# Performance work log

Hardware: AMD Instinct MI355X
Metric: run time of the kernel (lower is better)

## Reference

```python
import jax, jax.numpy as jnp
import numpy as np

L, D, H, HID, V, MAXLEN = 4, 768, 12, 3072, 32000, 1024
HD = D // H

def _pe_table(max_len, d_model):
    pos = np.arange(max_len)[:, None].astype(np.float64)
    i = np.arange(d_model)[None, :]
    ang = pos / np.power(10000.0, 2 * (i // 2) / d_model)
    ang[:, 0::2] = np.sin(ang[:, 0::2])
    ang[:, 1::2] = np.cos(ang[:, 1::2])
    return jnp.asarray(ang, dtype=jnp.float32)

def _layernorm(x, g, b, eps=1e-5):
    mu = jnp.mean(x, axis=-1, keepdims=True)
    var = jnp.mean(jnp.square(x - mu), axis=-1, keepdims=True)
    return (x - mu) * jax.lax.rsqrt(var + eps) * g + b

def setup_inputs() -> dict:
    key = jax.random.key(0)
    ks = jax.random.split(key, 16)
    s = 0.02
    inp = {
        'tokens': jax.random.randint(ks[0], (4, 1024), 0, V),
        'emb': jax.random.normal(ks[1], (V, D), jnp.float32) * s,
        'pe': _pe_table(MAXLEN, D),
        'ln1_g': jnp.ones((L, D), jnp.float32), 'ln1_b': jnp.zeros((L, D), jnp.float32),
        'wq': jax.random.normal(ks[2], (L, D, D), jnp.float32) * s, 'bq': jnp.zeros((L, D), jnp.float32),
        'wk': jax.random.normal(ks[3], (L, D, D), jnp.float32) * s, 'bk': jnp.zeros((L, D), jnp.float32),
        'wv': jax.random.normal(ks[4], (L, D, D), jnp.float32) * s, 'bv': jnp.zeros((L, D), jnp.float32),
        'wo': jax.random.normal(ks[5], (L, D, D), jnp.float32) * s, 'bo': jnp.zeros((L, D), jnp.float32),
        'ln2_g': jnp.ones((L, D), jnp.float32), 'ln2_b': jnp.zeros((L, D), jnp.float32),
        'w1': jax.random.normal(ks[6], (L, D, HID), jnp.float32) * s, 'b1': jnp.zeros((L, HID), jnp.float32),
        'w2': jax.random.normal(ks[7], (L, HID, D), jnp.float32) * s, 'b2': jnp.zeros((L, D), jnp.float32),
        'lnf_g': jnp.ones((D,), jnp.float32), 'lnf_b': jnp.zeros((D,), jnp.float32),
        'w_out': jax.random.normal(ks[8], (D, V), jnp.float32) * s,
    }
    return inp

def reference(tokens, emb, pe, ln1_g, ln1_b, wq, bq, wk, bk, wv, bv, wo, bo, ln2_g, ln2_b, w1, b1, w2, b2, lnf_g, lnf_b, w_out):
    B, S = tokens.shape
    x = emb[tokens] + pe[:S]  # [B,S,D]
    causal = jnp.tril(jnp.ones((S, S), bool))  # True = keep
    scale = 1.0 / jnp.sqrt(jnp.float32(D))  # NOTE: module scales by sqrt(d_model), not sqrt(head_dim)
    for l in range(L):
        h = _layernorm(x, ln1_g[l], ln1_b[l])
        def heads(w, b):
            return (h @ w + b).reshape(B, S, H, HD).transpose(0, 2, 1, 3)  # [B,H,S,HD]
        q, k, v = heads(wq[l], bq[l]), heads(wk[l], bk[l]), heads(wv[l], bv[l])
        scores = jnp.einsum('bhqd,bhkd->bhqk', q, k) * scale
        scores = jnp.where(causal, scores, -jnp.inf)
        probs = jax.nn.softmax(scores, axis=-1)
        attn = jnp.einsum('bhqk,bhkd->bhqd', probs, v)
        attn = attn.transpose(0, 2, 1, 3).reshape(B, S, D)
        x = x + attn @ wo[l] + bo[l]
        h2 = _layernorm(x, ln2_g[l], ln2_b[l])
        x = x + jax.nn.relu(h2 @ w1[l] + b1[l]) @ w2[l] + b2[l]
    hs = _layernorm(x, lnf_g, lnf_b)
    return hs @ w_out  # [B,S,V]
```

## Files before the change

### kernel.cpp

```cpp
#include <hip/hip_runtime.h>


typedef __bf16 bf16_t;
typedef bf16_t bf16x8 __attribute__((ext_vector_type(8)));
typedef bf16_t bf16x4 __attribute__((ext_vector_type(4)));
typedef float f32x4 __attribute__((ext_vector_type(4)));

#define GLD16(G, L) __builtin_amdgcn_global_load_lds(                          \
    (const __attribute__((address_space(1))) unsigned int*)(const void*)(G),   \
    (__attribute__((address_space(3))) unsigned int*)(void*)(L), 16, 0, 0)

__device__ __forceinline__ f32x4 mfma16(bf16x8 a, bf16x8 b, f32x4 c) {
  return __builtin_amdgcn_mfma_f32_16x16x32_bf16(a, b, c, 0, 0, 0);
}

__device__ __forceinline__ void barrier_raw() {
  asm volatile("s_barrier" ::: "memory");
}

__device__ __forceinline__ void lgkm0() {
  asm volatile("s_waitcnt lgkmcnt(0)" ::: "memory");
}

#define RED16_MAX(x) { x = fmaxf(x, __shfl_xor(x, 1)); x = fmaxf(x, __shfl_xor(x, 2)); \
                       x = fmaxf(x, __shfl_xor(x, 4)); x = fmaxf(x, __shfl_xor(x, 8)); }
#define RED16_SUM(x) { x += __shfl_xor(x, 1); x += __shfl_xor(x, 2); \
                       x += __shfl_xor(x, 4); x += __shfl_xor(x, 8); }

__device__ __forceinline__ int SW64(int row, int col) {
  return row * 64 + (col ^ ((row & 7) << 3));
}

__global__ __launch_bounds__(256)
void tconv_k(const float* __restrict__ in, bf16_t* __restrict__ out, int K, int N,
             size_t in_ls, size_t out_ls) {
  __shared__ float tile[32][33];
  in  += (size_t)blockIdx.z * in_ls;
  out += (size_t)blockIdx.z * out_ls;
  const int n0 = blockIdx.x * 32, k0 = blockIdx.y * 32;
  const int tx = threadIdx.x & 31, ty = threadIdx.x >> 5;
#pragma unroll
  for (int j = 0; j < 4; ++j)
    tile[ty + j * 8][tx] = in[(size_t)(k0 + ty + j * 8) * N + n0 + tx];
  __syncthreads();
#pragma unroll
  for (int j = 0; j < 4; ++j)
    out[(size_t)(n0 + ty + j * 8) * K + k0 + tx] = (bf16_t)tile[tx][ty + j * 8];
}

__global__ void qkvbias_k(const float* __restrict__ bq, const float* __restrict__ bk,
                          const float* __restrict__ bv, float* __restrict__ out) {
  const int l = blockIdx.x;
  for (int j = threadIdx.x; j < 2304; j += 256) {
    float v = (j < 768) ? bq[l * 768 + j]
            : (j < 1536) ? bk[l * 768 + j - 768]
                         : bv[l * 768 + j - 1536];
    out[l * 2304 + j] = v;
  }
}

__global__ __launch_bounds__(256)
void embed_k(const int* __restrict__ tok, const float* __restrict__ emb,
             const float* __restrict__ pe, float* __restrict__ xf) {
  const int row = blockIdx.x, tid = threadIdx.x;
  const int s = row & 1023;
  const int t = tok[row];
  float* o = xf + (size_t)row * 768;
  const float* e = emb + (size_t)t * 768;
  const float* p = pe + (size_t)s * 768;
  o[tid]       = e[tid]       + p[tid];
  o[tid + 256] = e[tid + 256] + p[tid + 256];
  o[tid + 512] = e[tid + 512] + p[tid + 512];
}

__global__ __launch_bounds__(256)
void ln_k(const float* __restrict__ x, const float* __restrict__ g,
          const float* __restrict__ bb, bf16_t* __restrict__ out) {
  const int wave = threadIdx.x >> 6, lane = threadIdx.x & 63;
  const int row = blockIdx.x * 4 + wave;
  const float* xr = x + (size_t)row * 768;
  f32x4 v[3];
#pragma unroll
  for (int c = 0; c < 3; ++c) v[c] = *(const f32x4*)&xr[c * 256 + lane * 4];
  float s = 0.0f;
#pragma unroll
  for (int c = 0; c < 3; ++c)
#pragma unroll
    for (int i = 0; i < 4; ++i) s += v[c][i];
#pragma unroll
  for (int off = 32; off; off >>= 1) s += __shfl_xor(s, off);
  const float mu = s * (1.0f / 768.0f);
  float s2 = 0.0f;
#pragma unroll
  for (int c = 0; c < 3; ++c)
#pragma unroll
    for (int i = 0; i < 4; ++i) {
      const float d = v[c][i] - mu;
      s2 += d * d;
    }
#pragma unroll
  for (int off = 32; off; off >>= 1) s2 += __shfl_xor(s2, off);
  const float rstd = rsqrtf(s2 * (1.0f / 768.0f) + 1e-5f);
  bf16_t* orow = out + (size_t)row * 768;
#pragma unroll
  for (int c = 0; c < 3; ++c) {
    const f32x4 gv = *(const f32x4*)&g[c * 256 + lane * 4];
    const f32x4 bv = *(const f32x4*)&bb[c * 256 + lane * 4];
    bf16x4 o;
#pragma unroll
    for (int i = 0; i < 4; ++i)
      o[i] = (bf16_t)((v[c][i] - mu) * rstd * gv[i] + bv[i]);
    *(bf16x4*)&orow[c * 256 + lane * 4] = o;
  }
}

template <bool BIAS, bool RELU, bool OUTF32, bool NT, int SUPER>
__global__ __launch_bounds__(512, 2)
void gemm8p(const bf16_t* __restrict__ A, const bf16_t* __restrict__ BT,
            const float* __restrict__ bias,
            float* __restrict__ outF, bf16_t* __restrict__ outB,
            int M, int N, int K) {
  extern __shared__ char smem[];
  const int NT_TILES = K >> 6;
  const int tilesM = M >> 8;
  const int cpx = gridDim.x >> 3;
  const int blk = ((int)blockIdx.x & 7) * cpx + ((int)blockIdx.x >> 3);
  int tm, tn;
  if (SUPER > 0) {
    const int grp = SUPER * tilesM;
    const int g = blk / grp, r = blk % grp;
    tm = r / SUPER;
    tn = g * SUPER + r % SUPER;
  } else {
    tm = blk % tilesM;
    tn = blk / tilesM;
  }
  const int tid = threadIdx.x;
  const int lane = tid & 63, wave = tid >> 6;
  const int wr = wave >> 2, wc = wave & 3;
  const int lrow = lane & 15, koct = lane >> 4;

  const size_t rowK = (size_t)K * 2;
  const int srow = tid >> 3;
  const int cswz = ((tid & 7) ^ (srow & 7)) << 4;
  const char* gA = (const char*)(A + (size_t)tm * 256 * K) + (size_t)srow * rowK + cswz;
  const char* gB = (const char*)(BT + (size_t)tn * 256 * K) + (size_t)srow * rowK + cswz;

  const int swz = (lrow & 7) << 4;
  const int aB0 = (wr * 128 + lrow) * 128 + ((koct * 16) ^ swz);
  const int bB0 = 32768 + (wc * 64 + lrow) * 128 + ((koct * 16) ^ swz);

  auto stageA = [&](int t) {
    char* d = smem + ((t & 1) << 16);
    const size_t kb = (size_t)t * 128;
    GLD16(gA + kb,              d + tid * 16);
    GLD16(gA + 64 * rowK + kb,  d + 8192 + tid * 16);
    GLD16(gA + 128 * rowK + kb, d + 16384 + tid * 16);
    GLD16(gA + 192 * rowK + kb, d + 24576 + tid * 16);
  };
  auto stageB = [&](int t) {
    char* d = smem + ((t & 1) << 16) + 32768;
    const size_t kb = (size_t)t * 128;
    GLD16(gB + kb,              d + tid * 16);
    GLD16(gB + 64 * rowK + kb,  d + 8192 + tid * 16);
    GLD16(gB + 128 * rowK + kb, d + 16384 + tid * 16);
    GLD16(gB + 192 * rowK + kb, d + 24576 + tid * 16);
  };

  stageA(0); stageB(0);
  stageA(1); stageB(1);

  f32x4 acc[8][4] = {};

  for (int t = 0; t < NT_TILES; ++t) {
    const char* rb = smem + ((t & 1) << 16);
    const bool pf = (t + 2) < NT_TILES;
    if (t == NT_TILES - 1) asm volatile("s_waitcnt vmcnt(0)" ::: "memory");
    else                   asm volatile("s_waitcnt vmcnt(8)" ::: "memory");
    barrier_raw();

    bf16x8 a0[4][2], a1[4][2], b[4][2];
#pragma unroll
    for (int mi = 0; mi < 4; ++mi) {
      const int o = aB0 + mi * 2048;
      a0[mi][0] = *(const bf16x8*)(rb + o);
      a0[mi][1] = *(const bf16x8*)(rb + (o ^ 64));
    }
#pragma unroll
    for (int ni = 0; ni < 2; ++ni) {
      const int o = bB0 + ni * 2048;
      b[ni][0] = *(const bf16x8*)(rb + o);
      b[ni][1] = *(const bf16x8*)(rb + (o ^ 64));
    }
    barrier_raw();
    lgkm0();
    __builtin_amdgcn_s_setprio(1);
#pragma unroll
    for (int mi = 0; mi < 4; ++mi)
#pragma unroll
      for (int ni = 0; ni < 2; ++ni) {
        acc[mi][ni] = mfma16(a0[mi][0], b[ni][0], acc[mi][ni]);
        acc[mi][ni] = mfma16(a0[mi][1], b[ni][1], acc[mi][ni]);
      }
    __builtin_amdgcn_s_setprio(0);
    barrier_raw();

#pragma unroll
    for (int ni = 2; ni < 4; ++ni) {
      const int o = bB0 + ni * 2048;
      b[ni][0] = *(const bf16x8*)(rb + o);
      b[ni][1] = *(const bf16x8*)(rb + (o ^ 64));
    }
    barrier_raw();
    lgkm0();
    __builtin_amdgcn_s_setprio(1);
#pragma unroll
    for (int mi = 0; mi < 4; ++mi)
#pragma unroll
      for (int ni = 2; ni < 4; ++ni) {
        acc[mi][ni] = mfma16(a0[mi][0], b[ni][0], acc[mi][ni]);
        acc[mi][ni] = mfma16(a0[mi][1], b[ni][1], acc[mi][ni]);
      }
    __builtin_amdgcn_s_setprio(0);
    barrier_raw();

    if (pf) stageB(t + 2);
#pragma unroll
    for (int mi = 0; mi < 4; ++mi) {
      const int o = aB0 + (mi + 4) * 2048;
      a1[mi][0] = *(const bf16x8*)(rb + o);
      a1[mi][1] = *(const bf16x8*)(rb + (o ^ 64));
    }
    barrier_raw();
    lgkm0();
    __builtin_amdgcn_s_setprio(1);
#pragma unroll
    for (int mi = 0; mi < 4; ++mi)
#pragma unroll
      for (int ni = 0; ni < 2; ++ni) {
        acc[mi + 4][ni] = mfma16(a1[mi][0], b[ni][0], acc[mi + 4][ni]);
        acc[mi + 4][ni] = mfma16(a1[mi][1], b[ni][1], acc[mi + 4][ni]);
      }
    __builtin_amdgcn_s_setprio(0);
    barrier_raw();

    if (pf) stageA(t + 2);
    barrier_raw();
    __builtin_amdgcn_s_setprio(1);
#pragma unroll
    for (int mi = 0; mi < 4; ++mi)
#pragma unroll
      for (int ni = 2; ni < 4; ++ni) {
        acc[mi + 4][ni] = mfma16(a1[mi][0], b[ni][0], acc[mi + 4][ni]);
        acc[mi + 4][ni] = mfma16(a1[mi][1], b[ni][1], acc[mi + 4][ni]);
      }
    __builtin_amdgcn_s_setprio(0);
  }

  barrier_raw();
  const int row0 = tm * 256 + wr * 128, col0 = tn * 256 + wc * 64;
  float bv[4];
#pragma unroll
  for (int ni = 0; ni < 4; ++ni)
    bv[ni] = BIAS ? bias[col0 + ni * 16 + lrow] : 0.0f;

  if (OUTF32) {
    float* lf = (float*)smem + wave * (32 * 68);
#pragma unroll
    for (int ph = 0; ph < 4; ++ph) {
#pragma unroll
      for (int mm = 0; mm < 2; ++mm) {
        const int mi = ph * 2 + mm;
#pragma unroll
        for (int ni = 0; ni < 4; ++ni)
#pragma unroll
          for (int r = 0; r < 4; ++r) {
            float v = acc[mi][ni][r] + bv[ni];
            if (RELU) v = fmaxf(v, 0.0f);
            lf[(mm * 16 + koct * 4 + r) * 68 + ni * 16 + lrow] = v;
          }
      }
#pragma unroll
      for (int j = 0; j < 8; ++j) {
        const int lr = j * 4 + koct;
        const int lc = lrow * 4;
        f32x4 v4 = *(const f32x4*)&lf[lr * 68 + lc];
        f32x4* dst = (f32x4*)&outF[(size_t)(row0 + ph * 32 + lr) * N + col0 + lc];
        if (NT) __builtin_nontemporal_store(v4, dst);
        else    *dst = v4;
      }
    }
  } else {
    bf16_t* lb = (bf16_t*)smem + wave * (32 * 72);
#pragma unroll
    for (int ph = 0; ph < 4; ++ph) {
#pragma unroll
      for (int mm = 0; mm < 2; ++mm) {
        const int mi = ph * 2 + mm;
#pragma unroll
        for (int ni = 0; ni < 4; ++ni)
#pragma unroll
          for (int r = 0; r < 4; ++r) {
            float v = acc[mi][ni][r] + bv[ni];
            if (RELU) v = fmaxf(v, 0.0f);
            lb[(mm * 16 + koct * 4 + r) * 72 + ni * 16 + lrow] = (bf16_t)v;
          }
      }
#pragma unroll
      for (int j = 0; j < 4; ++j) {
        const int lr = j * 8 + (lane >> 3);
        const int lc = (lane & 7) * 8;
        bf16x8 v8 = *(const bf16x8*)&lb[lr * 72 + lc];
        *(bf16x8*)&outB[(size_t)(row0 + ph * 32 + lr) * N + col0 + lc] = v8;
      }
    }
  }
}

template <bool BIAS, bool RELU, bool RESID, bool OUTF32>
__global__ __launch_bounds__(256, 2)
void gemmS(const bf16_t* __restrict__ A, const bf16_t* __restrict__ BT,
           const float* __restrict__ bias, const float* __restrict__ resid,
           float* __restrict__ outF, bf16_t* __restrict__ outB,
           int M, int N, int K) {
  extern __shared__ char smem[];
  const int NT = K >> 6;
  const int tiles_n = N >> 7;
  const int tm = blockIdx.x / tiles_n, tn = blockIdx.x % tiles_n;
  const int tid = threadIdx.x;
  const int wave = tid >> 6, lane = tid & 63;
  const int wr = wave >> 1, wc = wave & 1;
  const int lrow = lane & 15, koct = lane >> 4;

  const char* gA[2];
  const char* gB[4];
  {
    const char* Ab = (const char*)(A + (size_t)tm * 64 * K);
    const char* Bb = (const char*)(BT + (size_t)tn * 128 * K);
#pragma unroll
    for (int i = 0; i < 2; ++i) {
      const int off = i * 4096 + tid * 16;
      const int row = off >> 7;
      const int src = off ^ ((row & 7) << 4);
      gA[i] = Ab + (size_t)row * (2 * K) + (src & 127);
    }
#pragma unroll
    for (int i = 0; i < 4; ++i) {
      const int off = i * 4096 + tid * 16;
      const int row = off >> 7;
      const int src = off ^ ((row & 7) << 4);
      gB[i] = Bb + (size_t)row * (2 * K) + (src & 127);
    }
  }

  int aoff[2][2], boff[2][4];
#pragma unroll
  for (int kk = 0; kk < 2; ++kk) {
#pragma unroll
    for (int mi = 0; mi < 2; ++mi) {
      const int row = wr * 32 + mi * 16 + lrow;
      aoff[kk][mi] = (row * 128 + kk * 64 + koct * 16) ^ ((lrow & 7) << 4);
    }
#pragma unroll
    for (int ni = 0; ni < 4; ++ni) {
      const int row = wc * 64 + ni * 16 + lrow;
      boff[kk][ni] = 8192 + ((row * 128 + kk * 64 + koct * 16) ^ ((lrow & 7) << 4));
    }
  }

#pragma unroll
  for (int t = 0; t < 2; ++t) {
    char* sb = smem + t * 24576;
    const size_t kb = (size_t)t * 128;
    GLD16(gA[0] + kb, sb + tid * 16);
    GLD16(gA[1] + kb, sb + 4096 + tid * 16);
    GLD16(gB[0] + kb, sb + 8192 + tid * 16);
    GLD16(gB[1] + kb, sb + 12288 + tid * 16);
    GLD16(gB[2] + kb, sb + 16384 + tid * 16);
    GLD16(gB[3] + kb, sb + 20480 + tid * 16);
  }

  f32x4 acc[2][4] = {};

  for (int t = 0; t < NT; ++t) {
    char* sb = smem + (t % 3) * 24576;
    char* sb2 = smem + ((t + 2) % 3) * 24576;
    const bool pf = (t + 2) < NT;
    const size_t kb2 = (size_t)(t + 2) * 128;

    if (t == NT - 1) asm volatile("s_waitcnt vmcnt(0)" ::: "memory");
    else             asm volatile("s_waitcnt vmcnt(6)" ::: "memory");
    barrier_raw();

#pragma unroll
    for (int kk = 0; kk < 2; ++kk) {
      bf16x8 af[2], bfr[4];
#pragma unroll
      for (int mi = 0; mi < 2; ++mi)
        af[mi] = *(const bf16x8*)(sb + aoff[kk][mi]);
#pragma unroll
      for (int ni = 0; ni < 4; ++ni)
        bfr[ni] = *(const bf16x8*)(sb + boff[kk][ni]);
      if (pf) {
        if (kk == 0) {
          GLD16(gA[0] + kb2, sb2 + tid * 16);
          GLD16(gA[1] + kb2, sb2 + 4096 + tid * 16);
          GLD16(gB[0] + kb2, sb2 + 8192 + tid * 16);
        } else {
          GLD16(gB[1] + kb2, sb2 + 12288 + tid * 16);
          GLD16(gB[2] + kb2, sb2 + 16384 + tid * 16);
          GLD16(gB[3] + kb2, sb2 + 20480 + tid * 16);
        }
      }
      barrier_raw();
      __builtin_amdgcn_s_setprio(1);
#pragma unroll
      for (int mi = 0; mi < 2; ++mi)
#pragma unroll
        for (int ni = 0; ni < 4; ++ni)
          acc[mi][ni] = mfma16(af[mi], bfr[ni], acc[mi][ni]);
      __builtin_amdgcn_s_setprio(0);
    }
  }

  const int row0 = tm * 64 + wr * 32, col0 = tn * 128 + wc * 64;
#pragma unroll
  for (int ni = 0; ni < 4; ++ni) {
    const int col = col0 + ni * 16 + lrow;
    const float bv = BIAS ? bias[col] : 0.0f;
#pragma unroll
    for (int mi = 0; mi < 2; ++mi) {
#pragma unroll
      for (int r = 0; r < 4; ++r) {
        const int row = row0 + mi * 16 + koct * 4 + r;
        float v = acc[mi][ni][r] + bv;
        if (RELU) v = fmaxf(v, 0.0f);
        const size_t idx = (size_t)row * N + col;
        if (RESID) v += resid[idx];
        if (OUTF32) outF[idx] = v;
        else        outB[idx] = (bf16_t)v;
      }
    }
  }
}

__global__ __launch_bounds__(256)
void attn_k(const bf16_t* __restrict__ qkv, bf16_t* __restrict__ ab) {
  __shared__ __align__(16) bf16_t Qs[64 * 64];
  __shared__ __align__(16) bf16_t Ks[64 * 64];
  __shared__ __align__(16) bf16_t Vt[64 * 64];
  __shared__ __align__(16) bf16_t Ps[4][16 * 64];
  const int qt = blockIdx.x, h = blockIdx.y, b = blockIdx.z;
  const int tid = threadIdx.x;
  const int wave = tid >> 6, lane = tid & 63;
  const int lrow = lane & 15, koct = lane >> 4;
  const float scale = 0.03608439182435161f;

  const size_t RS = 2304;
  const bf16_t* qbase = qkv + h * 64;
  const bf16_t* kbase = qkv + 768 + h * 64;
  const bf16_t* vbase = qkv + 1536 + h * 64;

  const int sr = tid >> 3;
  const int sc = (((tid & 7) ^ (sr & 7)) << 3);

  {
#pragma unroll
    for (int i = 0; i < 2; ++i)
      GLD16(qbase + (size_t)(b * 1024 + qt * 64 + i * 32 + sr) * RS + sc,
            Qs + i * 2048 + tid * 8);
  }
  __syncthreads();
  bf16x8 qf[2];
  qf[0] = *(const bf16x8*)&Qs[SW64(wave * 16 + lrow, koct * 8)];
  qf[1] = *(const bf16x8*)&Qs[SW64(wave * 16 + lrow, 32 + koct * 8)];

  float m_r[4], l_r[4];
  f32x4 o[4] = {};
#pragma unroll
  for (int r = 0; r < 4; ++r) { m_r[r] = -1e30f; l_r[r] = 0.0f; }

  for (int kt = 0; kt <= qt; ++kt) {
    __syncthreads();
    {
#pragma unroll
      for (int i = 0; i < 2; ++i)
        GLD16(kbase + (size_t)(b * 1024 + kt * 64 + i * 32 + sr) * RS + sc,
              Ks + i * 2048 + tid * 8);
    }
    {
      const int kvr = lane;
      const int d0 = wave * 16;
      const bf16_t* vr = vbase + (size_t)(b * 1024 + kt * 64 + kvr) * RS + d0;
      bf16x8 v0 = *(const bf16x8*)vr;
      bf16x8 v1 = *(const bf16x8*)(vr + 8);
#pragma unroll
      for (int j = 0; j < 8; ++j) {
        Vt[(d0 + j) * 64 + (kvr ^ (j << 3))]     = v0[j];
        Vt[(d0 + 8 + j) * 64 + (kvr ^ (j << 3))] = v1[j];
      }
    }
    __syncthreads();

    f32x4 s[4] = {};
#pragma unroll
    for (int ni = 0; ni < 4; ++ni) {
      bf16x8 kf0 = *(const bf16x8*)&Ks[SW64(ni * 16 + lrow, koct * 8)];
      bf16x8 kf1 = *(const bf16x8*)&Ks[SW64(ni * 16 + lrow, 32 + koct * 8)];
      s[ni] = mfma16(qf[0], kf0, s[ni]);
      s[ni] = mfma16(qf[1], kf1, s[ni]);
    }

    const int qrow = qt * 64 + wave * 16 + koct * 4;
    float rm[4];
#pragma unroll
    for (int r = 0; r < 4; ++r) rm[r] = -1e30f;
#pragma unroll
    for (int ni = 0; ni < 4; ++ni) {
      const int kcol = kt * 64 + ni * 16 + lrow;
#pragma unroll
      for (int r = 0; r < 4; ++r) {
        float v = s[ni][r] * scale;
        if (kcol > qrow + r) v = -1e30f;
        s[ni][r] = v;
        rm[r] = fmaxf(rm[r], v);
      }
    }
#pragma unroll
    for (int r = 0; r < 4; ++r) RED16_MAX(rm[r]);
    float corr[4], ps[4];
#pragma unroll
    for (int r = 0; r < 4; ++r) {
      const float mn = fmaxf(m_r[r], rm[r]);
      corr[r] = __expf(m_r[r] - mn);
      m_r[r] = mn;
      ps[r] = 0.0f;
    }
#pragma unroll
    for (int ni = 0; ni < 4; ++ni)
#pragma unroll
      for (int r = 0; r < 4; ++r) {
        const float p = __expf(s[ni][r] - m_r[r]);
        s[ni][r] = p;
        ps[r] += p;
      }
#pragma unroll
    for (int r = 0; r < 4; ++r) RED16_SUM(ps[r]);
#pragma unroll
    for (int r = 0; r < 4; ++r) l_r[r] = l_r[r] * corr[r] + ps[r];
#pragma unroll
    for (int ni = 0; ni < 4; ++ni)
#pragma unroll
      for (int r = 0; r < 4; ++r) o[ni][r] *= corr[r];

#pragma unroll
    for (int ni = 0; ni < 4; ++ni)
#pragma unroll
      for (int r = 0; r < 4; ++r) {
        const int prow = koct * 4 + r;
        Ps[wave][prow * 64 + ((ni * 16 + lrow) ^ ((prow & 7) << 3))] =
            (bf16_t)s[ni][r];
      }
    __syncthreads();

    bf16x8 pa0 = *(const bf16x8*)&Ps[wave][SW64(lrow, koct * 8)];
    bf16x8 pa1 = *(const bf16x8*)&Ps[wave][SW64(lrow, 32 + koct * 8)];
#pragma unroll
    for (int ni = 0; ni < 4; ++ni) {
      bf16x8 vf0 = *(const bf16x8*)&Vt[SW64(ni * 16 + lrow, koct * 8)];
      bf16x8 vf1 = *(const bf16x8*)&Vt[SW64(ni * 16 + lrow, 32 + koct * 8)];
      o[ni] = mfma16(pa0, vf0, o[ni]);
      o[ni] = mfma16(pa1, vf1, o[ni]);
    }
  }

#pragma unroll
  for (int r = 0; r < 4; ++r) {
    const float inv = 1.0f / l_r[r];
    const int row = qt * 64 + wave * 16 + koct * 4 + r;
#pragma unroll
    for (int ni = 0; ni < 4; ++ni)
      ab[(size_t)(b * 1024 + row) * 768 + h * 64 + ni * 16 + lrow] =
          (bf16_t)(o[ni][r] * inv);
  }
}

extern "C" void kernel_launch(void* const* d_in, const int* in_sizes, int n_in,
                              void* d_out, int out_size, void* d_ws, size_t ws_size,
                              hipStream_t stream) {
  (void)in_sizes; (void)n_in; (void)out_size; (void)ws_size;
  const int*   tok   = (const int*)d_in[0];
  const float* emb   = (const float*)d_in[1];
  const float* pe    = (const float*)d_in[2];
  const float* ln1_g = (const float*)d_in[3];
  const float* ln1_b = (const float*)d_in[4];
  const float* wq    = (const float*)d_in[5];
  const float* bq    = (const float*)d_in[6];
  const float* wk    = (const float*)d_in[7];
  const float* bk    = (const float*)d_in[8];
  const float* wv    = (const float*)d_in[9];
  const float* bv    = (const float*)d_in[10];
  const float* wo    = (const float*)d_in[11];
  const float* bo    = (const float*)d_in[12];
  const float* ln2_g = (const float*)d_in[13];
  const float* ln2_b = (const float*)d_in[14];
  const float* w1    = (const float*)d_in[15];
  const float* b1    = (const float*)d_in[16];
  const float* w2    = (const float*)d_in[17];
  const float* b2    = (const float*)d_in[18];
  const float* lnf_g = (const float*)d_in[19];
  const float* lnf_b = (const float*)d_in[20];
  const float* w_out = (const float*)d_in[21];
  float* out = (float*)d_out;

  char* ws = (char*)d_ws;
  size_t off = 0;
  auto alloc = [&](size_t bytes) -> void* {
    void* p = ws + off;
    off += (bytes + 255) & ~(size_t)255;
    return p;
  };
  float*  xf      = (float*)alloc(4096ull * 768 * 4);
  bf16_t* hb      = (bf16_t*)alloc(4096ull * 768 * 2);
  bf16_t* qkvb    = (bf16_t*)alloc(4096ull * 2304 * 2);
  bf16_t* ab      = (bf16_t*)alloc(4096ull * 768 * 2);
  bf16_t* fb      = (bf16_t*)alloc(4096ull * 3072 * 2);
  float*  qkvbias = (float*)alloc(4ull * 2304 * 4);
  bf16_t* wqkvT   = (bf16_t*)alloc(4ull * 2304 * 768 * 2);
  bf16_t* woT     = (bf16_t*)alloc(4ull * 768 * 768 * 2);
  bf16_t* w1T     = (bf16_t*)alloc(4ull * 3072 * 768 * 2);
  bf16_t* w2T     = (bf16_t*)alloc(4ull * 768 * 3072 * 2);
  bf16_t* woutT   = (bf16_t*)alloc(32000ull * 768 * 2);

  tconv_k<<<dim3(24, 24, 4), 256, 0, stream>>>(wq, wqkvT, 768, 768,
      768ull * 768, 2304ull * 768);
  tconv_k<<<dim3(24, 24, 4), 256, 0, stream>>>(wk, wqkvT + 768ull * 768, 768, 768,
      768ull * 768, 2304ull * 768);
  tconv_k<<<dim3(24, 24, 4), 256, 0, stream>>>(wv, wqkvT + 2ull * 768 * 768, 768, 768,
      768ull * 768, 2304ull * 768);
  tconv_k<<<dim3(24, 24, 4), 256, 0, stream>>>(wo, woT, 768, 768,
      768ull * 768, 768ull * 768);
  tconv_k<<<dim3(96, 24, 4), 256, 0, stream>>>(w1, w1T, 768, 3072,
      768ull * 3072, 3072ull * 768);
  tconv_k<<<dim3(24, 96, 4), 256, 0, stream>>>(w2, w2T, 3072, 768,
      3072ull * 768, 768ull * 3072);
  tconv_k<<<dim3(1000, 24, 1), 256, 0, stream>>>(w_out, woutT, 768, 32000, 0, 0);
  qkvbias_k<<<4, 256, 0, stream>>>(bq, bk, bv, qkvbias);

  embed_k<<<4096, 256, 0, stream>>>(tok, emb, pe, xf);

  const size_t SMEM8P = 131072;
  const size_t SMEMS  = 3 * 24576;
  for (int l = 0; l < 4; ++l) {
    ln_k<<<1024, 256, 0, stream>>>(xf, ln1_g + l * 768, ln1_b + l * 768, hb);
    gemm8p<true, false, false, false, 0><<<16 * 9, 512, SMEM8P, stream>>>(
        hb, wqkvT + (size_t)l * 2304 * 768, qkvbias + l * 2304,
        nullptr, qkvb, 4096, 2304, 768);
    attn_k<<<dim3(16, 12, 4), 256, 0, stream>>>(qkvb, ab);
    gemmS<true, false, true, true><<<64 * 6, 256, SMEMS, stream>>>(
        ab, woT + (size_t)l * 768 * 768, bo + l * 768,
        xf, xf, nullptr, 4096, 768, 768);
    ln_k<<<1024, 256, 0, stream>>>(xf, ln2_g + l * 768, ln2_b + l * 768, hb);
    gemm8p<true, true, false, false, 0><<<16 * 12, 512, SMEM8P, stream>>>(
        hb, w1T + (size_t)l * 3072 * 768, b1 + l * 3072,
        nullptr, fb, 4096, 3072, 768);
    gemmS<true, false, true, true><<<64 * 6, 256, SMEMS, stream>>>(
        fb, w2T + (size_t)l * 768 * 3072, b2 + l * 768,
        xf, xf, nullptr, 4096, 768, 3072);
  }
  ln_k<<<1024, 256, 0, stream>>>(xf, lnf_g, lnf_b, hb);
  gemm8p<false, false, true, true, 5><<<16 * 125, 512, SMEM8P, stream>>>(
      hb, woutT, nullptr, out, nullptr, 4096, 32000, 768);
}
```

Before: 992.0 us.

## Enlarge attention query tile, trim GEMM barriers, use 2D block swizzle for logits

The attention kernel now processes 128 query rows per block with 8 waves, so each K/V tile is loaded once and shared across twice as many query rows, halving grid size and K/V traffic. In the main GEMM, several barriers and LDS waits between fragment loads and MFMA stages are removed or moved after the MFMA block, aiming to overlap LDS reads with compute. The logits GEMM changes from a 1D supergroup tile mapping to a 4x5 2D swizzle for better L2 reuse. The removed barriers risk LDS races if the staging order does not protect buffers, and the causal loop now runs over 64-key tiles up to the 128-row boundary, so upper waves do some wasted masked work.

```diff
diff --git a/kernel.cpp b/kernel.cpp
--- a/kernel.cpp
+++ b/kernel.cpp
@@ -114,7 +114,7 @@
   }
 }
 
-template <bool BIAS, bool RELU, bool OUTF32, bool NT, int SUPER>
+template <bool BIAS, bool RELU, bool OUTF32, bool NT, int SWM, int SWN>
 __global__ __launch_bounds__(512, 2)
 void gemm8p(const bf16_t* __restrict__ A, const bf16_t* __restrict__ BT,
             const float* __restrict__ bias,
@@ -126,11 +126,12 @@
   const int cpx = gridDim.x >> 3;
   const int blk = ((int)blockIdx.x & 7) * cpx + ((int)blockIdx.x >> 3);
   int tm, tn;
-  if (SUPER > 0) {
-    const int grp = SUPER * tilesM;
-    const int g = blk / grp, r = blk % grp;
-    tm = r / SUPER;
-    tn = g * SUPER + r % SUPER;
+  if (SWM > 0) {
+    const int g = blk / (SWM * SWN), r = blk % (SWM * SWN);
+    const int gmn = tilesM / SWM;
+    const int gm = g % gmn, gn = g / gmn;
+    tm = gm * SWM + (r % SWM);
+    tn = gn * SWN + (r / SWM);
   } else {
     tm = blk % tilesM;
     tn = blk / tilesM;
@@ -193,7 +194,6 @@
       b[ni][1] = *(const bf16x8*)(rb + (o ^ 64));
     }
     barrier_raw();
-    lgkm0();
     __builtin_amdgcn_s_setprio(1);
 #pragma unroll
     for (int mi = 0; mi < 4; ++mi)
@@ -211,8 +211,6 @@
       b[ni][0] = *(const bf16x8*)(rb + o);
       b[ni][1] = *(const bf16x8*)(rb + (o ^ 64));
     }
-    barrier_raw();
-    lgkm0();
     __builtin_amdgcn_s_setprio(1);
 #pragma unroll
     for (int mi = 0; mi < 4; ++mi)
@@ -222,6 +220,7 @@
         acc[mi][ni] = mfma16(a0[mi][1], b[ni][1], acc[mi][ni]);
       }
     __builtin_amdgcn_s_setprio(0);
+    lgkm0();
     barrier_raw();
 
     if (pf) stageB(t + 2);
@@ -231,8 +230,6 @@
       a1[mi][0] = *(const bf16x8*)(rb + o);
       a1[mi][1] = *(const bf16x8*)(rb + (o ^ 64));
     }
-    barrier_raw();
-    lgkm0();
     __builtin_amdgcn_s_setprio(1);
 #pragma unroll
     for (int mi = 0; mi < 4; ++mi)
@@ -242,10 +239,10 @@
         acc[mi + 4][ni] = mfma16(a1[mi][1], b[ni][1], acc[mi + 4][ni]);
       }
     __builtin_amdgcn_s_setprio(0);
+    lgkm0();
     barrier_raw();
 
     if (pf) stageA(t + 2);
-    barrier_raw();
     __builtin_amdgcn_s_setprio(1);
 #pragma unroll
     for (int mi = 0; mi < 4; ++mi)
@@ -444,12 +441,12 @@
   }
 }
 
-__global__ __launch_bounds__(256)
+__global__ __launch_bounds__(512)
 void attn_k(const bf16_t* __restrict__ qkv, bf16_t* __restrict__ ab) {
-  __shared__ __align__(16) bf16_t Qs[64 * 64];
+  __shared__ __align__(16) bf16_t Qs[128 * 64];
   __shared__ __align__(16) bf16_t Ks[64 * 64];
   __shared__ __align__(16) bf16_t Vt[64 * 64];
-  __shared__ __align__(16) bf16_t Ps[4][16 * 64];
+  __shared__ __align__(16) bf16_t Ps[8][16 * 64];
   const int qt = blockIdx.x, h = blockIdx.y, b = blockIdx.z;
   const int tid = threadIdx.x;
   const int wave = tid >> 6, lane = tid & 63;
@@ -467,8 +464,8 @@
   {
 #pragma unroll
     for (int i = 0; i < 2; ++i)
-      GLD16(qbase + (size_t)(b * 1024 + qt * 64 + i * 32 + sr) * RS + sc,
-            Qs + i * 2048 + tid * 8);
+      GLD16(qbase + (size_t)(b * 1024 + qt * 128 + i * 64 + sr) * RS + sc,
+            Qs + i * 4096 + tid * 8);
   }
   __syncthreads();
   bf16x8 qf[2];
@@ -480,25 +477,18 @@
 #pragma unroll
   for (int r = 0; r < 4; ++r) { m_r[r] = -1e30f; l_r[r] = 0.0f; }
 
-  for (int kt = 0; kt <= qt; ++kt) {
+  const int ktmax = 2 * qt + 1;
+  for (int kt = 0; kt <= ktmax; ++kt) {
     __syncthreads();
-    {
-#pragma unroll
-      for (int i = 0; i < 2; ++i)
-        GLD16(kbase + (size_t)(b * 1024 + kt * 64 + i * 32 + sr) * RS + sc,
-              Ks + i * 2048 + tid * 8);
-    }
+    GLD16(kbase + (size_t)(b * 1024 + kt * 64 + sr) * RS + sc, Ks + tid * 8);
     {
       const int kvr = lane;
-      const int d0 = wave * 16;
+      const int d0 = wave * 8;
       const bf16_t* vr = vbase + (size_t)(b * 1024 + kt * 64 + kvr) * RS + d0;
       bf16x8 v0 = *(const bf16x8*)vr;
-      bf16x8 v1 = *(const bf16x8*)(vr + 8);
-#pragma unroll
-      for (int j = 0; j < 8; ++j) {
-        Vt[(d0 + j) * 64 + (kvr ^ (j << 3))]     = v0[j];
-        Vt[(d0 + 8 + j) * 64 + (kvr ^ (j << 3))] = v1[j];
-      }
+#pragma unroll
+      for (int j = 0; j < 8; ++j)
+        Vt[(d0 + j) * 64 + (kvr ^ (((d0 + j) & 7) << 3))] = v0[j];
     }
     __syncthreads();
 
@@ -511,7 +501,7 @@
       s[ni] = mfma16(qf[1], kf1, s[ni]);
     }
 
-    const int qrow = qt * 64 + wave * 16 + koct * 4;
+    const int qrow = qt * 128 + wave * 16 + koct * 4;
     float rm[4];
 #pragma unroll
     for (int r = 0; r < 4; ++r) rm[r] = -1e30f;
@@ -577,7 +567,7 @@
 #pragma unroll
   for (int r = 0; r < 4; ++r) {
     const float inv = 1.0f / l_r[r];
-    const int row = qt * 64 + wave * 16 + koct * 4 + r;
+    const int row = qt * 128 + wave * 16 + koct * 4 + r;
 #pragma unroll
     for (int ni = 0; ni < 4; ++ni)
       ab[(size_t)(b * 1024 + row) * 768 + h * 64 + ni * 16 + lrow] =
@@ -653,15 +643,15 @@
   const size_t SMEMS  = 3 * 24576;
   for (int l = 0; l < 4; ++l) {
     ln_k<<<1024, 256, 0, stream>>>(xf, ln1_g + l * 768, ln1_b + l * 768, hb);
-    gemm8p<true, false, false, false, 0><<<16 * 9, 512, SMEM8P, stream>>>(
+    gemm8p<true, false, false, false, 0, 0><<<16 * 9, 512, SMEM8P, stream>>>(
         hb, wqkvT + (size_t)l * 2304 * 768, qkvbias + l * 2304,
         nullptr, qkvb, 4096, 2304, 768);
-    attn_k<<<dim3(16, 12, 4), 256, 0, stream>>>(qkvb, ab);
+    attn_k<<<dim3(8, 12, 4), 512, 0, stream>>>(qkvb, ab);
     gemmS<true, false, true, true><<<64 * 6, 256, SMEMS, stream>>>(
         ab, woT + (size_t)l * 768 * 768, bo + l * 768,
         xf, xf, nullptr, 4096, 768, 768);
     ln_k<<<1024, 256, 0, stream>>>(xf, ln2_g + l * 768, ln2_b + l * 768, hb);
-    gemm8p<true, true, false, false, 0><<<16 * 12, 512, SMEM8P, stream>>>(
+    gemm8p<true, true, false, false, 0, 0><<<16 * 12, 512, SMEM8P, stream>>>(
         hb, w1T + (size_t)l * 3072 * 768, b1 + l * 3072,
         nullptr, fb, 4096, 3072, 768);
     gemmS<true, false, true, true><<<64 * 6, 256, SMEMS, stream>>>(
@@ -669,6 +659,6 @@
         xf, xf, nullptr, 4096, 768, 3072);
   }
   ln_k<<<1024, 256, 0, stream>>>(xf, lnf_g, lnf_b, hb);
-  gemm8p<false, false, true, true, 5><<<16 * 125, 512, SMEM8P, stream>>>(
+  gemm8p<false, false, true, true, 4, 5><<<16 * 125, 512, SMEM8P, stream>>>(
       hb, woutT, nullptr, out, nullptr, 4096, 32000, 768);
 }
```

New measurement: 1.006 ms. Within noise of the previous version (+1.4%).
